# Optimization experiments

Measured on AMD Instinct MI355X. Metric: run time of the kernel, lower is better.

The kernel has to match this reference:

```python
import jax, jax.numpy as jnp
import numpy as np

N_DRUG = 50000
N_DIS = 50000
D = 128      # input feature dim (lazily inferred by GCNConv(-1, h))
H = 128      # hidden_channels
OUT = 64     # out_channels
E = 800000   # edges per relation
L = 2        # num_layers
NUM_REL = 4  # [drug-drug, dis-dis, drug->dis, dis->drug]


def setup_inputs() -> dict:
    key = jax.random.key(0)
    ks = jax.random.split(key, 10)
    x_drug = jax.random.normal(ks[0], (N_DRUG, D), jnp.float32)
    x_dis = jax.random.normal(ks[1], (N_DIS, D), jnp.float32)
    ei_dd = jax.random.randint(ks[2], (2, E), 0, N_DRUG, dtype=jnp.int32)
    ei_ss = jax.random.randint(ks[3], (2, E), 0, N_DIS, dtype=jnp.int32)
    ei_ds = jax.random.randint(ks[4], (2, E), 0, N_DRUG, dtype=jnp.int32)  # row<N_DRUG, col<N_DIS (equal sizes)
    ei_sd = jax.random.randint(ks[5], (2, E), 0, N_DIS, dtype=jnp.int32)
    # per-layer, per-relation GCN weights (glorot-ish scale) and biases
    Ws = jax.random.normal(ks[6], (L, NUM_REL, D, H), jnp.float32) * (1.0 / np.sqrt(D))
    bs = jnp.zeros((L, NUM_REL, H), jnp.float32)
    lin_w = jax.random.normal(ks[7], (OUT, H), jnp.float32) * (1.0 / np.sqrt(H))
    lin_b = jnp.zeros((OUT,), jnp.float32)
    return {"x_drug": x_drug, "x_dis": x_dis, "ei_dd": ei_dd, "ei_ss": ei_ss,
            "ei_ds": ei_ds, "ei_sd": ei_sd, "Ws": Ws, "bs": bs,
            "lin_w": lin_w, "lin_b": lin_b}


def _gcn(x_src, ei, n_src, n_dst, W, b, self_loops):
    """GCNConv: symmetric degree-normalized gather -> scatter-add -> linear."""
    row, col = ei[0], ei[1]
    if self_loops:  # homogeneous relation: add self loops (n_src == n_dst)
        idx = jnp.arange(n_dst, dtype=row.dtype)
        row = jnp.concatenate([row, idx])
        col = jnp.concatenate([col, idx])
    ones = jnp.ones(row.shape[0], x_src.dtype)
    deg_s = jax.ops.segment_sum(ones, row, num_segments=n_src)
    deg_d = jax.ops.segment_sum(ones, col, num_segments=n_dst)
    dinv_s = jnp.where(deg_s > 0, jax.lax.rsqrt(jnp.maximum(deg_s, 1.0)), 0.0)
    dinv_d = jnp.where(deg_d > 0, jax.lax.rsqrt(jnp.maximum(deg_d, 1.0)), 0.0)
    norm = dinv_s[row] * dinv_d[col]                      # [E]
    h = x_src @ W                                         # [n_src, H]
    out = jax.ops.segment_sum(h[row] * norm[:, None], col, num_segments=n_dst)
    return out + b


def reference(x_drug, x_dis, ei_dd, ei_ss, ei_ds, ei_sd, Ws, bs, lin_w, lin_b):
    for l in range(L):
        drug_new = (_gcn(x_drug, ei_dd, N_DRUG, N_DRUG, Ws[l, 0], bs[l, 0], True)
                    + _gcn(x_dis, ei_sd, N_DIS, N_DRUG, Ws[l, 3], bs[l, 3], False))
        dis_new = (_gcn(x_dis, ei_ss, N_DIS, N_DIS, Ws[l, 1], bs[l, 1], True)
                   + _gcn(x_drug, ei_ds, N_DRUG, N_DIS, Ws[l, 2], bs[l, 2], False))
        x_drug = jax.nn.relu(drug_new)
        x_dis = jax.nn.relu(dis_new)
    return (x_drug @ lin_w.T + lin_b, x_dis @ lin_w.T + lin_b)
```

## Files before the change

kernel.cpp:

```cpp
#include <hip/hip_runtime.h>

#define NV   50000
#define FD   128
#define NE   800000
#define NOUT 64
#define NBIN 196
#define CH   2048
#define NBLK 391
#define SCAN_L (NBIN * NBLK)
#define SCHUNK 2048
#define NSCH ((SCAN_L + SCHUNK - 1) / SCHUNK)
#define CAP2 12288

typedef unsigned short bf16_t;
typedef unsigned char  u8;
typedef __attribute__((ext_vector_type(8))) short bf16x8;
typedef __attribute__((ext_vector_type(4))) float f32x4;

__device__ __forceinline__ bf16_t f2bf(float f) {
  unsigned u = __builtin_bit_cast(unsigned, f);
  return (bf16_t)((u + 0x7fffu + ((u >> 16) & 1u)) >> 16);
}
__device__ __forceinline__ float bflo(unsigned v) { return __builtin_bit_cast(float, v << 16); }
__device__ __forceinline__ float bfhi(unsigned v) { return __builtin_bit_cast(float, v & 0xffff0000u); }
__device__ __forceinline__ unsigned pk2(float a, float b) {
  return (unsigned)f2bf(a) | ((unsigned)f2bf(b) << 16);
}

struct Ptr4 { const int* p[4]; };


__global__ __launch_bounds__(256) void p0_hist(Ptr4 rows, Ptr4 cols,
                                               int* __restrict__ blockCnt) {
  const int r = blockIdx.y, blk = blockIdx.x, t = threadIdx.x;
  __shared__ int cd[NBIN], cs[NBIN];
  for (int i = t; i < NBIN; i += 256) { cd[i] = 0; cs[i] = 0; }
  __syncthreads();
  const int e0 = blk * CH;
  const int n4 = min(CH, NE - e0) >> 2;
  const int4* rw4 = (const int4*)(rows.p[r] + e0);
  const int4* cl4 = (const int4*)(cols.p[r] + e0);
  for (int i = t; i < n4; i += 256) {
    int4 a = cl4[i], b = rw4[i];
    atomicAdd(&cd[a.x >> 8], 1); atomicAdd(&cd[a.y >> 8], 1);
    atomicAdd(&cd[a.z >> 8], 1); atomicAdd(&cd[a.w >> 8], 1);
    atomicAdd(&cs[b.x >> 8], 1); atomicAdd(&cs[b.y >> 8], 1);
    atomicAdd(&cs[b.z >> 8], 1); atomicAdd(&cs[b.w >> 8], 1);
  }
  __syncthreads();
  int* bd = blockCnt + (size_t)(r * 2 + 0) * SCAN_L;
  int* bs = blockCnt + (size_t)(r * 2 + 1) * SCAN_L;
  for (int i = t; i < NBIN; i += 256) {
    bd[i * NBLK + blk] = cd[i];
    bs[i * NBLK + blk] = cs[i];
  }
}

__global__ __launch_bounds__(256) void scan_pass1(const int* __restrict__ blockCnt,
                                                  int* __restrict__ chunkSum) {
  const int r2 = blockIdx.y, chunk = blockIdx.x, t = threadIdx.x;
  const int* a = blockCnt + (size_t)r2 * SCAN_L + chunk * SCHUNK;
  const int n = min(SCHUNK, SCAN_L - chunk * SCHUNK);
  int s = 0;
  for (int i = t; i < n; i += 256) s += a[i];
  __shared__ int sm[256];
  sm[t] = s;
  __syncthreads();
  #pragma unroll
  for (int off = 128; off > 0; off >>= 1) {
    if (t < off) sm[t] += sm[t + off];
    __syncthreads();
  }
  if (t == 0) chunkSum[r2 * NSCH + chunk] = sm[0];
}

__global__ __launch_bounds__(512) void scan_pass2(int* __restrict__ chunkSum,
                                                  int* __restrict__ bucketBase) {
  const int t = threadIdx.x;
  __shared__ int sm[8 * NSCH];
  if (t < 8 * NSCH) sm[t] = chunkSum[t];
  __syncthreads();
  if (t < 8) {
    int run = 0;
    for (int j = 0; j < NSCH; ++j) {
      int v = sm[t * NSCH + j];
      sm[t * NSCH + j] = run;
      run += v;
    }
    bucketBase[t * (NBIN + 1) + NBIN] = NE;
  }
  __syncthreads();
  if (t < 8 * NSCH) chunkSum[t] = sm[t];
}

__global__ __launch_bounds__(256) void scan_pass3(int* __restrict__ blockCnt,
                                                  const int* __restrict__ chunkSum,
                                                  int* __restrict__ bucketBase) {
  const int r2 = blockIdx.y, chunk = blockIdx.x, t = threadIdx.x;
  int* a = blockCnt + (size_t)r2 * SCAN_L + chunk * SCHUNK;
  const int gbase = chunk * SCHUNK;
  const int n = min(SCHUNK, SCAN_L - gbase);
  const int idx0 = t * 8;
  int v[8];
  int s = 0;
  #pragma unroll
  for (int j = 0; j < 8; ++j) {
    int id = idx0 + j;
    v[j] = (id < n) ? a[id] : 0;
    s += v[j];
  }
  __shared__ int sm[256];
  sm[t] = s;
  __syncthreads();
  for (int off = 1; off < 256; off <<= 1) {
    int x = (t >= off) ? sm[t - off] : 0;
    __syncthreads();
    sm[t] += x;
    __syncthreads();
  }
  int pre = ((t == 0) ? 0 : sm[t - 1]) + chunkSum[r2 * NSCH + chunk];
  #pragma unroll
  for (int j = 0; j < 8; ++j) {
    int id = idx0 + j;
    if (id < n) {
      int val = v[j];
      a[id] = pre;
      int g = gbase + id;
      if (g % NBLK == 0) bucketBase[r2 * (NBIN + 1) + g / NBLK] = pre;
      pre += val;
    }
  }
}

__global__ __launch_bounds__(256) void p1_scatter(Ptr4 rows, Ptr4 cols,
                                                  const int* __restrict__ blockCnt,
                                                  unsigned* __restrict__ pairD,
                                                  u8* __restrict__ srcb) {
  const int r = blockIdx.y, blk = blockIdx.x, t = threadIdx.x;
  const int e0 = blk * CH;
  const int n = min(CH, NE - e0);
  const int* rw = rows.p[r] + e0;
  const int* cl = cols.p[r] + e0;

  __shared__ int sc[256], lofs[256], cnt2[256], baseT[256];
  __shared__ unsigned pr[CH];
  __shared__ u8 binb[CH];
  __shared__ u8 pay8[CH];

  {
    const int* win = blockCnt + (size_t)(r * 2 + 0) * SCAN_L;
    int c = 0;
    if (t < NBIN) {
      int idx = t * NBLK + blk;
      int base = win[idx];
      int nxt = (idx + 1 < SCAN_L) ? win[idx + 1] : NE;
      baseT[t] = base;
      c = nxt - base;
    }
    sc[t] = c;
    cnt2[t] = 0;
  }
  __syncthreads();
  for (int off = 1; off < 256; off <<= 1) {
    int v = (t >= off) ? sc[t - off] : 0;
    __syncthreads();
    sc[t] += v;
    __syncthreads();
  }
  lofs[t] = (t == 0) ? 0 : sc[t - 1];
  __syncthreads();
  for (int i = t; i < n; i += 256) {
    int c = cl[i];
    int bin = c >> 8;
    int rank = atomicAdd(&cnt2[bin], 1);
    int p = lofs[bin] + rank;
    pr[p] = ((unsigned)(c & 255) << 16) | (unsigned)rw[i];
    binb[p] = (u8)bin;
  }
  __syncthreads();
  {
    unsigned* pd = pairD + (size_t)r * NE;
    for (int i = t; i < n; i += 256) {
      int bin = binb[i];
      pd[baseT[bin] + (i - lofs[bin])] = pr[i];
    }
  }
  __syncthreads();

  {
    const int* win = blockCnt + (size_t)(r * 2 + 1) * SCAN_L;
    int c = 0;
    if (t < NBIN) {
      int idx = t * NBLK + blk;
      int base = win[idx];
      int nxt = (idx + 1 < SCAN_L) ? win[idx + 1] : NE;
      baseT[t] = base;
      c = nxt - base;
    }
    sc[t] = c;
    cnt2[t] = 0;
  }
  __syncthreads();
  for (int off = 1; off < 256; off <<= 1) {
    int v = (t >= off) ? sc[t - off] : 0;
    __syncthreads();
    sc[t] += v;
    __syncthreads();
  }
  lofs[t] = (t == 0) ? 0 : sc[t - 1];
  __syncthreads();
  for (int i = t; i < n; i += 256) {
    int sv = rw[i];
    int bin = sv >> 8;
    int rank = atomicAdd(&cnt2[bin], 1);
    int p = lofs[bin] + rank;
    pay8[p] = (u8)(sv & 255);
    binb[p] = (u8)bin;
  }
  __syncthreads();
  {
    u8* sb = srcb + (size_t)r * NE;
    for (int i = t; i < n; i += 256) {
      int bin = binb[i];
      sb[baseT[bin] + (i - lofs[bin])] = pay8[i];
    }
  }
}

__global__ __launch_bounds__(256) void p2_csr(const unsigned* __restrict__ pairD,
                                              const int* __restrict__ bucketBase,
                                              int* __restrict__ srcidx,
                                              int* __restrict__ rowptr,
                                              float* __restrict__ dinvD) {
  const int r = blockIdx.y, bin = blockIdx.x, t = threadIdx.x;
  const int* bb = bucketBase + (r * 2 + 0) * (NBIN + 1);
  const int base = bb[bin], next = bb[bin + 1];
  const int span = next - base;
  const unsigned* pd = pairD + (size_t)r * NE + base;

  __shared__ int cnt[256], sc[256], ex[256], cnt2[256];
  __shared__ int lsrc[CAP2];
  cnt[t] = 0; cnt2[t] = 0;
  __syncthreads();
  for (int i = t; i < span; i += 256) atomicAdd(&cnt[pd[i] >> 16], 1);
  __syncthreads();
  sc[t] = cnt[t];
  __syncthreads();
  for (int off = 1; off < 256; off <<= 1) {
    int v = (t >= off) ? sc[t - off] : 0;
    __syncthreads();
    sc[t] += v;
    __syncthreads();
  }
  ex[t] = (t == 0) ? 0 : sc[t - 1];
  __syncthreads();

  const int node = (bin << 8) + t;
  if (node < NV) {
    rowptr[r * (NV + 1) + node] = base + ex[t];
    float deg = (float)cnt[t];
    dinvD[r * NV + node] = (r < 2) ? rsqrtf(deg + 1.f)
                                   : (deg > 0.f ? rsqrtf(deg) : 0.f);
  }
  if (bin == NBIN - 1 && t == 0) rowptr[r * (NV + 1) + NV] = NE;

  int* so = srcidx + (size_t)r * NE + base;
  if (span <= CAP2) {
    for (int i = t; i < span; i += 256) {
      unsigned v = pd[i];
      int dl = v >> 16;
      int rank = atomicAdd(&cnt2[dl], 1);
      lsrc[ex[dl] + rank] = (int)(v & 0xFFFFu);
    }
    __syncthreads();
    for (int i = t; i < span; i += 256) so[i] = lsrc[i];
  } else {
    for (int i = t; i < span; i += 256) {
      unsigned v = pd[i];
      int dl = v >> 16;
      int rank = atomicAdd(&cnt2[dl], 1);
      so[ex[dl] + rank] = (int)(v & 0xFFFFu);
    }
  }
}

__global__ __launch_bounds__(256) void p2_srcdeg(const u8* __restrict__ srcb,
                                                 const int* __restrict__ bucketBase,
                                                 float* __restrict__ dinvS) {
  const int r = blockIdx.y, bin = blockIdx.x, t = threadIdx.x;
  const int* bb = bucketBase + (r * 2 + 1) * (NBIN + 1);
  const int base = bb[bin], next = bb[bin + 1];
  const int span = next - base;
  const u8* sb = srcb + (size_t)r * NE + base;
  __shared__ int cnt[256];
  cnt[t] = 0;
  __syncthreads();
  for (int i = t; i < span; i += 256) atomicAdd(&cnt[sb[i]], 1);
  __syncthreads();
  int node = (bin << 8) + t;
  if (node < NV) {
    float deg = (float)cnt[t];
    dinvS[r * NV + node] = (r < 2) ? rsqrtf(deg + 1.f)
                                   : (deg > 0.f ? rsqrtf(deg) : 0.f);
  }
}

__global__ __launch_bounds__(256) void wprep(const float* __restrict__ Wsrc,
                                             bf16_t* __restrict__ Wt) {
  int idx = blockIdx.x * 256 + threadIdx.x;
  if (idx < 8 * 128 * 128) {
    int i = idx >> 14, n = (idx >> 7) & 127, k = idx & 127;
    Wt[idx] = f2bf(Wsrc[(size_t)i * 16384 + k * 128 + n]);
  }
}

struct G4 {
  const void*   X[4];
  const bf16_t* W[4];
  const float*  dS[4];
  bf16_t*       H[4];
};

template<bool F32IN>
__global__ __launch_bounds__(256) void gemm_quad(G4 g) {
  const int q = blockIdx.y;
  const void* Xb = g.X[q]; const bf16_t* Wt = g.W[q];
  const float* dS = g.dS[q]; bf16_t* H = g.H[q];

  __shared__ bf16_t Xs[128][136];
  __shared__ bf16_t Wsh[128][136];
  __shared__ float sdS[128];
  const int t = threadIdx.x;
  const int row0 = blockIdx.x * 128;

  #pragma unroll
  for (int j = 0; j < 8; ++j) {
    int r = (t >> 4) + j * 16;
    int c = (t & 15) * 8;
    int gr = row0 + r;
    uint4 xv = make_uint4(0u, 0u, 0u, 0u);
    if (gr < NV) {
      if constexpr (F32IN) {
        const float* Xf = (const float*)Xb;
        float4 v0 = *(const float4*)(Xf + (size_t)gr * FD + c);
        float4 v1 = *(const float4*)(Xf + (size_t)gr * FD + c + 4);
        xv = make_uint4(pk2(v0.x, v0.y), pk2(v0.z, v0.w),
                        pk2(v1.x, v1.y), pk2(v1.z, v1.w));
      } else {
        xv = *(const uint4*)((const bf16_t*)Xb + (size_t)gr * FD + c);
      }
    }
    *(uint4*)&Xs[r][c] = xv;
    *(uint4*)&Wsh[r][c] = *(const uint4*)(Wt + (size_t)r * FD + c);
  }
  if (t < 128) {
    int gidx = row0 + t;
    sdS[t] = (gidx < NV) ? dS[gidx] : 0.f;
  }
  __syncthreads();

  const int wave = t >> 6, lane = t & 63;
  const int lr = lane & 15;
  const int lk = (lane >> 4) * 8;
  const int mb = wave * 32;

  f32x4 acc[2][8];
  #pragma unroll
  for (int m = 0; m < 2; ++m)
    #pragma unroll
    for (int n = 0; n < 8; ++n) acc[m][n] = (f32x4){0.f, 0.f, 0.f, 0.f};

  #pragma unroll
  for (int kc = 0; kc < 128; kc += 32) {
    bf16x8 a0 = *(const bf16x8*)&Xs[mb + lr][kc + lk];
    bf16x8 a1 = *(const bf16x8*)&Xs[mb + 16 + lr][kc + lk];
    bf16x8 b[8];
    #pragma unroll
    for (int n = 0; n < 8; ++n) b[n] = *(const bf16x8*)&Wsh[n * 16 + lr][kc + lk];
    #pragma unroll
    for (int n = 0; n < 8; ++n) {
      acc[0][n] = __builtin_amdgcn_mfma_f32_16x16x32_bf16(a0, b[n], acc[0][n], 0, 0, 0);
      acc[1][n] = __builtin_amdgcn_mfma_f32_16x16x32_bf16(a1, b[n], acc[1][n], 0, 0, 0);
    }
  }

  __syncthreads();
  const int rgrp = (lane >> 4) * 4;
  #pragma unroll
  for (int m = 0; m < 2; ++m)
    #pragma unroll
    for (int n = 0; n < 8; ++n)
      #pragma unroll
      for (int j = 0; j < 4; ++j) {
        int rr = mb + m * 16 + rgrp + j;
        Wsh[rr][n * 16 + lr] = f2bf(acc[m][n][j] * sdS[rr]);
      }
  __syncthreads();

  #pragma unroll
  for (int j = 0; j < 8; ++j) {
    int r = (t >> 4) + j * 16;
    int c = (t & 15) * 8;
    int gr = row0 + r;
    if (gr < NV) *(uint4*)(H + (size_t)gr * FD + c) = *(const uint4*)&Wsh[r][c];
  }
}

__device__ __forceinline__ void gather8(const bf16_t* __restrict__ h,
                                        const int* __restrict__ src,
                                        int p0, int p1, int d,
                                        float& ax, float& ay) {
  int p = p0;
  while (p + 8 <= p1) {
    int s0 = src[p + 0], s1 = src[p + 1], s2 = src[p + 2], s3 = src[p + 3];
    int s4 = src[p + 4], s5 = src[p + 5], s6 = src[p + 6], s7 = src[p + 7];
    unsigned v0 = *(const unsigned*)(h + (s0 << 7) + d);
    unsigned v1 = *(const unsigned*)(h + (s1 << 7) + d);
    unsigned v2 = *(const unsigned*)(h + (s2 << 7) + d);
    unsigned v3 = *(const unsigned*)(h + (s3 << 7) + d);
    unsigned v4 = *(const unsigned*)(h + (s4 << 7) + d);
    unsigned v5 = *(const unsigned*)(h + (s5 << 7) + d);
    unsigned v6 = *(const unsigned*)(h + (s6 << 7) + d);
    unsigned v7 = *(const unsigned*)(h + (s7 << 7) + d);
    ax += bflo(v0); ay += bfhi(v0);
    ax += bflo(v1); ay += bfhi(v1);
    ax += bflo(v2); ay += bfhi(v2);
    ax += bflo(v3); ay += bfhi(v3);
    ax += bflo(v4); ay += bfhi(v4);
    ax += bflo(v5); ay += bfhi(v5);
    ax += bflo(v6); ay += bfhi(v6);
    ax += bflo(v7); ay += bfhi(v7);
    p += 8;
  }
  while (p + 2 <= p1) {
    int s0 = src[p], s1 = src[p + 1];
    unsigned v0 = *(const unsigned*)(h + (s0 << 7) + d);
    unsigned v1 = *(const unsigned*)(h + (s1 << 7) + d);
    ax += bflo(v0); ay += bfhi(v0);
    ax += bflo(v1); ay += bfhi(v1);
    p += 2;
  }
  if (p < p1) {
    int s = src[p];
    unsigned v = *(const unsigned*)(h + (s << 7) + d);
    ax += bflo(v); ay += bfhi(v);
  }
}

struct PullSide {
  const bf16_t* hA; const int* rpA; const int* srcA; const float* dDA;
  const bf16_t* hB; const int* rpB; const int* srcB; const float* dDB;
  const float* bA; const float* bB; bf16_t* Y;
};

__global__ __launch_bounds__(256) void pull_dual(PullSide s0, PullSide s1) {
  const PullSide& a = blockIdx.y ? s1 : s0;
  const int i = __builtin_amdgcn_readfirstlane(blockIdx.x * 4 + (threadIdx.x >> 6));
  if (i >= NV) return;
  const int lane = threadIdx.x & 63;
  const int d = lane * 2;

  float ax, ay;
  {
    unsigned v = *(const unsigned*)(a.hA + (i << 7) + d);
    ax = bflo(v); ay = bfhi(v);
  }
  gather8(a.hA, a.srcA, a.rpA[i], a.rpA[i + 1], d, ax, ay);
  float bx = 0.f, by = 0.f;
  gather8(a.hB, a.srcB, a.rpB[i], a.rpB[i + 1], d, bx, by);

  float wA = a.dDA[i], wB = a.dDB[i];
  float ox = fmaf(ax, wA, fmaf(bx, wB, a.bA[d] + a.bB[d]));
  float oy = fmaf(ay, wA, fmaf(by, wB, a.bA[d + 1] + a.bB[d + 1]));
  *(unsigned*)(a.Y + (size_t)i * FD + d) = pk2(fmaxf(ox, 0.f), fmaxf(oy, 0.f));
}

__global__ __launch_bounds__(256) void linear64(const bf16_t* __restrict__ Xb,
                                                const float* __restrict__ lw,
                                                const float* __restrict__ lb,
                                                float* __restrict__ Out) {
  __shared__ float Wt[128][68];
  __shared__ float Xs[64][132];
  const int tid = threadIdx.x;
  const int row0 = blockIdx.x * 64;

  for (int i = tid * 4; i < 64 * 128; i += 1024) {
    float4 v = *(const float4*)(lw + i);
    int o = i >> 7, h = i & 127;
    Wt[h + 0][o] = v.x; Wt[h + 1][o] = v.y; Wt[h + 2][o] = v.z; Wt[h + 3][o] = v.w;
  }
  for (int i = tid * 8; i < 64 * 128; i += 2048) {
    int rr = i >> 7, cc = i & 127;
    int gr = row0 + rr;
    uint4 v = make_uint4(0u, 0u, 0u, 0u);
    if (gr < NV) v = *(const uint4*)(Xb + (size_t)gr * FD + cc);
    unsigned* pv = (unsigned*)&v;
    #pragma unroll
    for (int q = 0; q < 4; ++q) {
      Xs[rr][cc + q * 2]     = bflo(pv[q]);
      Xs[rr][cc + q * 2 + 1] = bfhi(pv[q]);
    }
  }
  __syncthreads();

  const int tx = tid & 15, ty = tid >> 4;
  float acc[4][4];
  #pragma unroll
  for (int i = 0; i < 4; ++i)
    #pragma unroll
    for (int j = 0; j < 4; ++j) acc[i][j] = 0.f;

  for (int k = 0; k < 128; k += 4) {
    float4 xr[4], w[4];
    #pragma unroll
    for (int i = 0; i < 4; ++i) xr[i] = *(const float4*)&Xs[ty * 4 + i][k];
    #pragma unroll
    for (int j = 0; j < 4; ++j) w[j] = *(const float4*)&Wt[k + j][tx * 4];
    #pragma unroll
    for (int i = 0; i < 4; ++i) {
      const float* xv = (const float*)&xr[i];
      #pragma unroll
      for (int j = 0; j < 4; ++j) {
        float x = xv[j];
        acc[i][0] = fmaf(x, w[j].x, acc[i][0]);
        acc[i][1] = fmaf(x, w[j].y, acc[i][1]);
        acc[i][2] = fmaf(x, w[j].z, acc[i][2]);
        acc[i][3] = fmaf(x, w[j].w, acc[i][3]);
      }
    }
  }
  float4 bias = *(const float4*)(lb + tx * 4);
  #pragma unroll
  for (int i = 0; i < 4; ++i) {
    int gr = row0 + ty * 4 + i;
    if (gr < NV) {
      *(float4*)(Out + (size_t)gr * NOUT + tx * 4) =
          make_float4(acc[i][0] + bias.x, acc[i][1] + bias.y,
                      acc[i][2] + bias.z, acc[i][3] + bias.w);
    }
  }
}


extern "C" void kernel_launch(void* const* d_in, const int* in_sizes, int n_in,
                              void* d_out, int out_size, void* d_ws, size_t ws_size,
                              hipStream_t stream) {
  const float* x_drug = (const float*)d_in[0];
  const float* x_dis  = (const float*)d_in[1];
  const int* ei[4] = { (const int*)d_in[2], (const int*)d_in[3],
                       (const int*)d_in[4], (const int*)d_in[5] };
  const float* Ws = (const float*)d_in[6];
  const float* bs = (const float*)d_in[7];
  const float* lw = (const float*)d_in[8];
  const float* lb = (const float*)d_in[9];
  float* out = (float*)d_out;

  char* p = (char*)d_ws;
  auto take = [&](size_t bytes) -> void* {
    char* q = p;
    p += (bytes + 255) & ~(size_t)255;
    return (void*)q;
  };
  int* blockCnt   = (int*)take((size_t)8 * SCAN_L * sizeof(int));
  int* chunkSum   = (int*)take((size_t)8 * NSCH * sizeof(int));
  int* bucketBase = (int*)take((size_t)8 * (NBIN + 1) * sizeof(int));
  unsigned* pairD = (unsigned*)take((size_t)4 * NE * sizeof(unsigned));
  u8* srcb        = (u8*)take((size_t)4 * NE);
  int* srcidx     = (int*)take((size_t)4 * NE * sizeof(int));
  int* rowptr     = (int*)take((size_t)4 * (NV + 1) * sizeof(int));
  float* dinvS    = (float*)take((size_t)4 * NV * sizeof(float));
  float* dinvD    = (float*)take((size_t)4 * NV * sizeof(float));
  bf16_t* hA  = (bf16_t*)take((size_t)NV * FD * sizeof(bf16_t));
  bf16_t* hB  = (bf16_t*)take((size_t)NV * FD * sizeof(bf16_t));
  bf16_t* hC  = (bf16_t*)take((size_t)NV * FD * sizeof(bf16_t));
  bf16_t* hD  = (bf16_t*)take((size_t)NV * FD * sizeof(bf16_t));
  bf16_t* Wtb = (bf16_t*)take((size_t)8 * FD * FD * sizeof(bf16_t));
  bf16_t* XD1 = (bf16_t*)take((size_t)NV * FD * sizeof(bf16_t));
  bf16_t* XS1 = (bf16_t*)take((size_t)NV * FD * sizeof(bf16_t));
  bf16_t* XD2 = (bf16_t*)take((size_t)NV * FD * sizeof(bf16_t));
  bf16_t* XS2 = (bf16_t*)take((size_t)NV * FD * sizeof(bf16_t));

  Ptr4 rows = {{ ei[0], ei[1], ei[2], ei[3] }};
  Ptr4 cols = {{ ei[0] + NE, ei[1] + NE, ei[2] + NE, ei[3] + NE }};

  p0_hist<<<dim3(NBLK, 4), 256, 0, stream>>>(rows, cols, blockCnt);
  scan_pass1<<<dim3(NSCH, 8), 256, 0, stream>>>(blockCnt, chunkSum);
  scan_pass2<<<1, 512, 0, stream>>>(chunkSum, bucketBase);
  scan_pass3<<<dim3(NSCH, 8), 256, 0, stream>>>(blockCnt, chunkSum, bucketBase);
  p1_scatter<<<dim3(NBLK, 4), 256, 0, stream>>>(rows, cols, blockCnt, pairD, srcb);
  p2_csr<<<dim3(NBIN, 4), 256, 0, stream>>>(pairD, bucketBase, srcidx, rowptr, dinvD);
  p2_srcdeg<<<dim3(NBIN, 4), 256, 0, stream>>>(srcb, bucketBase, dinvS);
  wprep<<<(8 * FD * FD + 255) / 256, 256, 0, stream>>>(Ws, Wtb);

  const dim3 GEMM_GRID((NV + 127) / 128, 4);
  const dim3 PULL_GRID((NV + 3) / 4, 2);
  const int LIN_GRID = (NV + 63) / 64;
  const void* xd = x_drug;
  const void* xs = x_dis;
  bf16_t* nextd[2] = {XD1, XD2};
  bf16_t* nexts[2] = {XS1, XS2};
  for (int l = 0; l < 2; ++l) {
    const bf16_t* W0 = Wtb + (size_t)(l * 4 + 0) * FD * FD;
    const bf16_t* W1 = Wtb + (size_t)(l * 4 + 1) * FD * FD;
    const bf16_t* W2 = Wtb + (size_t)(l * 4 + 2) * FD * FD;
    const bf16_t* W3 = Wtb + (size_t)(l * 4 + 3) * FD * FD;
    const float* b0 = bs + (l * 4 + 0) * FD;
    const float* b1 = bs + (l * 4 + 1) * FD;
    const float* b2 = bs + (l * 4 + 2) * FD;
    const float* b3 = bs + (l * 4 + 3) * FD;

    G4 g;
    g.X[0] = xd;  g.W[0] = W0; g.dS[0] = dinvS + 0 * NV; g.H[0] = hA;
    g.X[1] = xs;  g.W[1] = W3; g.dS[1] = dinvS + 3 * NV; g.H[1] = hB;
    g.X[2] = xs;  g.W[2] = W1; g.dS[2] = dinvS + 1 * NV; g.H[2] = hC;
    g.X[3] = xd;  g.W[3] = W2; g.dS[3] = dinvS + 2 * NV; g.H[3] = hD;
    if (l == 0) gemm_quad<true><<<GEMM_GRID, 256, 0, stream>>>(g);
    else        gemm_quad<false><<<GEMM_GRID, 256, 0, stream>>>(g);

    PullSide pd_;
    pd_.hA = hA; pd_.rpA = rowptr + 0 * (NV + 1); pd_.srcA = srcidx + (size_t)0 * NE;
    pd_.dDA = dinvD + 0 * NV;
    pd_.hB = hB; pd_.rpB = rowptr + 3 * (NV + 1); pd_.srcB = srcidx + (size_t)3 * NE;
    pd_.dDB = dinvD + 3 * NV;
    pd_.bA = b0; pd_.bB = b3; pd_.Y = nextd[l];
    PullSide ps_;
    ps_.hA = hC; ps_.rpA = rowptr + 1 * (NV + 1); ps_.srcA = srcidx + (size_t)1 * NE;
    ps_.dDA = dinvD + 1 * NV;
    ps_.hB = hD; ps_.rpB = rowptr + 2 * (NV + 1); ps_.srcB = srcidx + (size_t)2 * NE;
    ps_.dDB = dinvD + 2 * NV;
    ps_.bA = b1; ps_.bB = b2; ps_.Y = nexts[l];
    pull_dual<<<PULL_GRID, 256, 0, stream>>>(pd_, ps_);

    xd = nextd[l];
    xs = nexts[l];
  }

  linear64<<<LIN_GRID, 256, 0, stream>>>((const bf16_t*)xd, lw, lb, out);
  linear64<<<LIN_GRID, 256, 0, stream>>>((const bf16_t*)xs, lw, lb, out + (size_t)NV * NOUT);
}
```

Before: 409.4 us.

## Share X tile across paired GEMMs and merge small launches

The GEMM kernel now loads each input tile once and multiplies it by both relation weights that consume the same node type, instead of loading X separately for each of four relations. The two p2 kernels are merged into one launch, and the two final linear launches are merged via a second grid dimension. The aim is to halve X reads for the GEMM and cut launch overhead. In exchange the GEMM uses more LDS per block (two weight tiles), which may lower occupancy, and it launches half as many blocks.

Measured after the change: 408.6 us. No clear change (-0.2%).

```diff
diff --git a/kernel.cpp b/kernel.cpp
--- a/kernel.cpp
+++ b/kernel.cpp
@@ -227,81 +227,83 @@
   }
 }
 
-__global__ __launch_bounds__(256) void p2_csr(const unsigned* __restrict__ pairD,
-                                              const int* __restrict__ bucketBase,
-                                              int* __restrict__ srcidx,
-                                              int* __restrict__ rowptr,
-                                              float* __restrict__ dinvD) {
+__global__ __launch_bounds__(256) void p2_build(const unsigned* __restrict__ pairD,
+                                                const u8* __restrict__ srcb,
+                                                const int* __restrict__ bucketBase,
+                                                int* __restrict__ srcidx,
+                                                int* __restrict__ rowptr,
+                                                float* __restrict__ dinvD,
+                                                float* __restrict__ dinvS) {
   const int r = blockIdx.y, bin = blockIdx.x, t = threadIdx.x;
-  const int* bb = bucketBase + (r * 2 + 0) * (NBIN + 1);
-  const int base = bb[bin], next = bb[bin + 1];
-  const int span = next - base;
-  const unsigned* pd = pairD + (size_t)r * NE + base;
-
   __shared__ int cnt[256], sc[256], ex[256], cnt2[256];
   __shared__ int lsrc[CAP2];
-  cnt[t] = 0; cnt2[t] = 0;
-  __syncthreads();
-  for (int i = t; i < span; i += 256) atomicAdd(&cnt[pd[i] >> 16], 1);
-  __syncthreads();
-  sc[t] = cnt[t];
-  __syncthreads();
-  for (int off = 1; off < 256; off <<= 1) {
-    int v = (t >= off) ? sc[t - off] : 0;
-    __syncthreads();
-    sc[t] += v;
-    __syncthreads();
-  }
-  ex[t] = (t == 0) ? 0 : sc[t - 1];
-  __syncthreads();
-
-  const int node = (bin << 8) + t;
-  if (node < NV) {
-    rowptr[r * (NV + 1) + node] = base + ex[t];
-    float deg = (float)cnt[t];
-    dinvD[r * NV + node] = (r < 2) ? rsqrtf(deg + 1.f)
-                                   : (deg > 0.f ? rsqrtf(deg) : 0.f);
-  }
-  if (bin == NBIN - 1 && t == 0) rowptr[r * (NV + 1) + NV] = NE;
-
-  int* so = srcidx + (size_t)r * NE + base;
-  if (span <= CAP2) {
-    for (int i = t; i < span; i += 256) {
-      unsigned v = pd[i];
-      int dl = v >> 16;
-      int rank = atomicAdd(&cnt2[dl], 1);
-      lsrc[ex[dl] + rank] = (int)(v & 0xFFFFu);
-    }
-    __syncthreads();
-    for (int i = t; i < span; i += 256) so[i] = lsrc[i];
-  } else {
-    for (int i = t; i < span; i += 256) {
-      unsigned v = pd[i];
-      int dl = v >> 16;
-      int rank = atomicAdd(&cnt2[dl], 1);
-      so[ex[dl] + rank] = (int)(v & 0xFFFFu);
-    }
-  }
-}
-
-__global__ __launch_bounds__(256) void p2_srcdeg(const u8* __restrict__ srcb,
-                                                 const int* __restrict__ bucketBase,
-                                                 float* __restrict__ dinvS) {
-  const int r = blockIdx.y, bin = blockIdx.x, t = threadIdx.x;
-  const int* bb = bucketBase + (r * 2 + 1) * (NBIN + 1);
-  const int base = bb[bin], next = bb[bin + 1];
-  const int span = next - base;
-  const u8* sb = srcb + (size_t)r * NE + base;
-  __shared__ int cnt[256];
-  cnt[t] = 0;
-  __syncthreads();
-  for (int i = t; i < span; i += 256) atomicAdd(&cnt[sb[i]], 1);
-  __syncthreads();
-  int node = (bin << 8) + t;
-  if (node < NV) {
-    float deg = (float)cnt[t];
-    dinvS[r * NV + node] = (r < 2) ? rsqrtf(deg + 1.f)
-                                   : (deg > 0.f ? rsqrtf(deg) : 0.f);
+
+  {
+    const int* bb = bucketBase + (r * 2 + 0) * (NBIN + 1);
+    const int base = bb[bin], next = bb[bin + 1];
+    const int span = next - base;
+    const unsigned* pd = pairD + (size_t)r * NE + base;
+
+    cnt[t] = 0; cnt2[t] = 0;
+    __syncthreads();
+    for (int i = t; i < span; i += 256) atomicAdd(&cnt[pd[i] >> 16], 1);
+    __syncthreads();
+    sc[t] = cnt[t];
+    __syncthreads();
+    for (int off = 1; off < 256; off <<= 1) {
+      int v = (t >= off) ? sc[t - off] : 0;
+      __syncthreads();
+      sc[t] += v;
+      __syncthreads();
+    }
+    ex[t] = (t == 0) ? 0 : sc[t - 1];
+    __syncthreads();
+
+    const int node = (bin << 8) + t;
+    if (node < NV) {
+      rowptr[r * (NV + 1) + node] = base + ex[t];
+      float deg = (float)cnt[t];
+      dinvD[r * NV + node] = (r < 2) ? rsqrtf(deg + 1.f)
+                                     : (deg > 0.f ? rsqrtf(deg) : 0.f);
+    }
+    if (bin == NBIN - 1 && t == 0) rowptr[r * (NV + 1) + NV] = NE;
+
+    int* so = srcidx + (size_t)r * NE + base;
+    if (span <= CAP2) {
+      for (int i = t; i < span; i += 256) {
+        unsigned v = pd[i];
+        int dl = v >> 16;
+        int rank = atomicAdd(&cnt2[dl], 1);
+        lsrc[ex[dl] + rank] = (int)(v & 0xFFFFu);
+      }
+      __syncthreads();
+      for (int i = t; i < span; i += 256) so[i] = lsrc[i];
+    } else {
+      for (int i = t; i < span; i += 256) {
+        unsigned v = pd[i];
+        int dl = v >> 16;
+        int rank = atomicAdd(&cnt2[dl], 1);
+        so[ex[dl] + rank] = (int)(v & 0xFFFFu);
+      }
+    }
+  }
+  __syncthreads();
+
+  {
+    const int* bb = bucketBase + (r * 2 + 1) * (NBIN + 1);
+    const int base = bb[bin], next = bb[bin + 1];
+    const int span = next - base;
+    const u8* sb = srcb + (size_t)r * NE + base;
+    cnt[t] = 0;
+    __syncthreads();
+    for (int i = t; i < span; i += 256) atomicAdd(&cnt[sb[i]], 1);
+    __syncthreads();
+    int node = (bin << 8) + t;
+    if (node < NV) {
+      float deg = (float)cnt[t];
+      dinvS[r * NV + node] = (r < 2) ? rsqrtf(deg + 1.f)
+                                     : (deg > 0.f ? rsqrtf(deg) : 0.f);
+    }
   }
 }
 
@@ -314,22 +316,19 @@
   }
 }
 
-struct G4 {
-  const void*   X[4];
-  const bf16_t* W[4];
-  const float*  dS[4];
-  bf16_t*       H[4];
+struct G2 {
+  const void*   X;
+  const bf16_t* Wa; const float* dSa; bf16_t* Ha;
+  const bf16_t* Wb; const float* dSb; bf16_t* Hb;
 };
 
 template<bool F32IN>
-__global__ __launch_bounds__(256) void gemm_quad(G4 g) {
-  const int q = blockIdx.y;
-  const void* Xb = g.X[q]; const bf16_t* Wt = g.W[q];
-  const float* dS = g.dS[q]; bf16_t* H = g.H[q];
+__global__ __launch_bounds__(256) void gemm_pairX(G2 g0, G2 g1) {
+  const G2& g = blockIdx.y ? g1 : g0;
 
   __shared__ bf16_t Xs[128][136];
-  __shared__ bf16_t Wsh[128][136];
-  __shared__ float sdS[128];
+  __shared__ bf16_t Wsh[2][128][136];
+  __shared__ float sdS[2][128];
   const int t = threadIdx.x;
   const int row0 = blockIdx.x * 128;
 
@@ -341,21 +340,23 @@
     uint4 xv = make_uint4(0u, 0u, 0u, 0u);
     if (gr < NV) {
       if constexpr (F32IN) {
-        const float* Xf = (const float*)Xb;
+        const float* Xf = (const float*)g.X;
         float4 v0 = *(const float4*)(Xf + (size_t)gr * FD + c);
         float4 v1 = *(const float4*)(Xf + (size_t)gr * FD + c + 4);
         xv = make_uint4(pk2(v0.x, v0.y), pk2(v0.z, v0.w),
                         pk2(v1.x, v1.y), pk2(v1.z, v1.w));
       } else {
-        xv = *(const uint4*)((const bf16_t*)Xb + (size_t)gr * FD + c);
+        xv = *(const uint4*)((const bf16_t*)g.X + (size_t)gr * FD + c);
       }
     }
     *(uint4*)&Xs[r][c] = xv;
-    *(uint4*)&Wsh[r][c] = *(const uint4*)(Wt + (size_t)r * FD + c);
+    *(uint4*)&Wsh[0][r][c] = *(const uint4*)(g.Wa + (size_t)r * FD + c);
+    *(uint4*)&Wsh[1][r][c] = *(const uint4*)(g.Wb + (size_t)r * FD + c);
   }
   if (t < 128) {
     int gidx = row0 + t;
-    sdS[t] = (gidx < NV) ? dS[gidx] : 0.f;
+    sdS[0][t] = (gidx < NV) ? g.dSa[gidx] : 0.f;
+    sdS[1][t] = (gidx < NV) ? g.dSb[gidx] : 0.f;
   }
   __syncthreads();
 
@@ -363,46 +364,50 @@
   const int lr = lane & 15;
   const int lk = (lane >> 4) * 8;
   const int mb = wave * 32;
-
-  f32x4 acc[2][8];
+  const int rgrp = (lane >> 4) * 4;
+
   #pragma unroll
-  for (int m = 0; m < 2; ++m)
-    #pragma unroll
-    for (int n = 0; n < 8; ++n) acc[m][n] = (f32x4){0.f, 0.f, 0.f, 0.f};
-
-  #pragma unroll
-  for (int kc = 0; kc < 128; kc += 32) {
-    bf16x8 a0 = *(const bf16x8*)&Xs[mb + lr][kc + lk];
-    bf16x8 a1 = *(const bf16x8*)&Xs[mb + 16 + lr][kc + lk];
-    bf16x8 b[8];
-    #pragma unroll
-    for (int n = 0; n < 8; ++n) b[n] = *(const bf16x8*)&Wsh[n * 16 + lr][kc + lk];
-    #pragma unroll
-    for (int n = 0; n < 8; ++n) {
-      acc[0][n] = __builtin_amdgcn_mfma_f32_16x16x32_bf16(a0, b[n], acc[0][n], 0, 0, 0);
-      acc[1][n] = __builtin_amdgcn_mfma_f32_16x16x32_bf16(a1, b[n], acc[1][n], 0, 0, 0);
-    }
-  }
-
-  __syncthreads();
-  const int rgrp = (lane >> 4) * 4;
-  #pragma unroll
-  for (int m = 0; m < 2; ++m)
-    #pragma unroll
-    for (int n = 0; n < 8; ++n)
+  for (int s = 0; s < 2; ++s) {
+    f32x4 acc[2][8];
+    #pragma unroll
+    for (int m = 0; m < 2; ++m)
       #pragma unroll
-      for (int j = 0; j < 4; ++j) {
-        int rr = mb + m * 16 + rgrp + j;
-        Wsh[rr][n * 16 + lr] = f2bf(acc[m][n][j] * sdS[rr]);
+      for (int n = 0; n < 8; ++n) acc[m][n] = (f32x4){0.f, 0.f, 0.f, 0.f};
+
+    #pragma unroll
+    for (int kc = 0; kc < 128; kc += 32) {
+      bf16x8 a0 = *(const bf16x8*)&Xs[mb + lr][kc + lk];
+      bf16x8 a1 = *(const bf16x8*)&Xs[mb + 16 + lr][kc + lk];
+      bf16x8 b[8];
+      #pragma unroll
+      for (int n = 0; n < 8; ++n) b[n] = *(const bf16x8*)&Wsh[s][n * 16 + lr][kc + lk];
+      #pragma unroll
+      for (int n = 0; n < 8; ++n) {
+        acc[0][n] = __builtin_amdgcn_mfma_f32_16x16x32_bf16(a0, b[n], acc[0][n], 0, 0, 0);
+        acc[1][n] = __builtin_amdgcn_mfma_f32_16x16x32_bf16(a1, b[n], acc[1][n], 0, 0, 0);
       }
-  __syncthreads();
-
-  #pragma unroll
-  for (int j = 0; j < 8; ++j) {
-    int r = (t >> 4) + j * 16;
-    int c = (t & 15) * 8;
-    int gr = row0 + r;
-    if (gr < NV) *(uint4*)(H + (size_t)gr * FD + c) = *(const uint4*)&Wsh[r][c];
+    }
+
+    __syncthreads();
+    #pragma unroll
+    for (int m = 0; m < 2; ++m)
+      #pragma unroll
+      for (int n = 0; n < 8; ++n)
+        #pragma unroll
+        for (int j = 0; j < 4; ++j) {
+          int rr = mb + m * 16 + rgrp + j;
+          Wsh[s][rr][n * 16 + lr] = f2bf(acc[m][n][j] * sdS[s][rr]);
+        }
+    __syncthreads();
+
+    bf16_t* H = s ? g.Hb : g.Ha;
+    #pragma unroll
+    for (int j = 0; j < 8; ++j) {
+      int r = (t >> 4) + j * 16;
+      int c = (t & 15) * 8;
+      int gr = row0 + r;
+      if (gr < NV) *(uint4*)(H + (size_t)gr * FD + c) = *(const uint4*)&Wsh[s][r][c];
+    }
   }
 }
 
@@ -475,10 +480,13 @@
   *(unsigned*)(a.Y + (size_t)i * FD + d) = pk2(fmaxf(ox, 0.f), fmaxf(oy, 0.f));
 }
 
-__global__ __launch_bounds__(256) void linear64(const bf16_t* __restrict__ Xb,
+__global__ __launch_bounds__(256) void linear64(const bf16_t* __restrict__ X0,
+                                                const bf16_t* __restrict__ X1,
                                                 const float* __restrict__ lw,
                                                 const float* __restrict__ lb,
                                                 float* __restrict__ Out) {
+  const bf16_t* Xb = blockIdx.y ? X1 : X0;
+  float* O = Out + (size_t)blockIdx.y * NV * NOUT;
   __shared__ float Wt[128][68];
   __shared__ float Xs[64][132];
   const int tid = threadIdx.x;
@@ -534,7 +542,7 @@
   for (int i = 0; i < 4; ++i) {
     int gr = row0 + ty * 4 + i;
     if (gr < NV) {
-      *(float4*)(Out + (size_t)gr * NOUT + tx * 4) =
+      *(float4*)(O + (size_t)gr * NOUT + tx * 4) =
           make_float4(acc[i][0] + bias.x, acc[i][1] + bias.y,
                       acc[i][2] + bias.z, acc[i][3] + bias.w);
     }
@@ -588,13 +596,13 @@
   scan_pass2<<<1, 512, 0, stream>>>(chunkSum, bucketBase);
   scan_pass3<<<dim3(NSCH, 8), 256, 0, stream>>>(blockCnt, chunkSum, bucketBase);
   p1_scatter<<<dim3(NBLK, 4), 256, 0, stream>>>(rows, cols, blockCnt, pairD, srcb);
-  p2_csr<<<dim3(NBIN, 4), 256, 0, stream>>>(pairD, bucketBase, srcidx, rowptr, dinvD);
-  p2_srcdeg<<<dim3(NBIN, 4), 256, 0, stream>>>(srcb, bucketBase, dinvS);
+  p2_build<<<dim3(NBIN, 4), 256, 0, stream>>>(pairD, srcb, bucketBase,
+                                              srcidx, rowptr, dinvD, dinvS);
   wprep<<<(8 * FD * FD + 255) / 256, 256, 0, stream>>>(Ws, Wtb);
 
-  const dim3 GEMM_GRID((NV + 127) / 128, 4);
+  const dim3 GEMM_GRID((NV + 127) / 128, 2);
   const dim3 PULL_GRID((NV + 3) / 4, 2);
-  const int LIN_GRID = (NV + 63) / 64;
+  const dim3 LIN_GRID((NV + 63) / 64, 2);
   const void* xd = x_drug;
   const void* xs = x_dis;
   bf16_t* nextd[2] = {XD1, XD2};
@@ -609,13 +617,13 @@
     const float* b2 = bs + (l * 4 + 2) * FD;
     const float* b3 = bs + (l * 4 + 3) * FD;
 
-    G4 g;
-    g.X[0] = xd;  g.W[0] = W0; g.dS[0] = dinvS + 0 * NV; g.H[0] = hA;
-    g.X[1] = xs;  g.W[1] = W3; g.dS[1] = dinvS + 3 * NV; g.H[1] = hB;
-    g.X[2] = xs;  g.W[2] = W1; g.dS[2] = dinvS + 1 * NV; g.H[2] = hC;
-    g.X[3] = xd;  g.W[3] = W2; g.dS[3] = dinvS + 2 * NV; g.H[3] = hD;
-    if (l == 0) gemm_quad<true><<<GEMM_GRID, 256, 0, stream>>>(g);
-    else        gemm_quad<false><<<GEMM_GRID, 256, 0, stream>>>(g);
+    G2 gd, gs;
+    gd.X = xd; gd.Wa = W0; gd.dSa = dinvS + 0 * NV; gd.Ha = hA;
+               gd.Wb = W2; gd.dSb = dinvS + 2 * NV; gd.Hb = hD;
+    gs.X = xs; gs.Wa = W1; gs.dSa = dinvS + 1 * NV; gs.Ha = hC;
+               gs.Wb = W3; gs.dSb = dinvS + 3 * NV; gs.Hb = hB;
+    if (l == 0) gemm_pairX<true><<<GEMM_GRID, 256, 0, stream>>>(gd, gs);
+    else        gemm_pairX<false><<<GEMM_GRID, 256, 0, stream>>>(gd, gs);
 
     PullSide pd_;
     pd_.hA = hA; pd_.rpA = rowptr + 0 * (NV + 1); pd_.srcA = srcidx + (size_t)0 * NE;
@@ -635,6 +643,6 @@
     xs = nexts[l];
   }
 
-  linear64<<<LIN_GRID, 256, 0, stream>>>((const bf16_t*)xd, lw, lb, out);
-  linear64<<<LIN_GRID, 256, 0, stream>>>((const bf16_t*)xs, lw, lb, out + (size_t)NV * NOUT);
-}
+  linear64<<<LIN_GRID, 256, 0, stream>>>((const bf16_t*)xd, (const bf16_t*)xs,
+                                         lw, lb, out);
+}
```
